# Kernel tuning notes

Hardware: AMD Instinct MI355X
Metric: run time of the kernel (lower is better)

The kernel has to match this reference:

```python
import jax, jax.numpy as jnp
import numpy as np

EPS = 1e-7  # K.epsilon()
ROUTINGS = 3


def squash(v, axis=-1):
    s2 = jnp.sum(jnp.square(v), axis=axis, keepdims=True)
    scale = s2 / (1.0 + s2) / jnp.sqrt(s2 + EPS)
    return scale * v


def setup_inputs() -> dict:
    key = jax.random.key(0)
    k1, k2 = jax.random.split(key)
    B, Ni, Di, No, Do = 64, 2048, 16, 32, 16
    inputs = jax.random.normal(k1, (B, Ni, Di), dtype=jnp.float32)
    # glorot-uniform-ish scale for W
    limit = np.sqrt(6.0 / (Di + Do)).astype(np.float32)
    W = jax.random.uniform(k2, (1, Ni, No, Do, Di), dtype=jnp.float32,
                           minval=-limit, maxval=limit)
    return {"inputs": inputs, "W": W}


def reference(inputs, W):
    # inputs: [B, Ni, Di]; W: [1, Ni, No, Do, Di]
    # inputs_hat[b,n,o,d] = sum_i W[n,o,d,i] * inputs[b,n,i]  -> [B, Ni, No, Do]
    inputs_hat = jnp.einsum('bni,nodi->bnod', inputs, W[0])
    B, Ni, No, _ = inputs_hat.shape
    b = jnp.zeros((B, Ni, No), dtype=inputs_hat.dtype)
    outputs = None
    for i in range(ROUTINGS):
        c = jax.nn.softmax(b, axis=2)              # [B, Ni, No]
        s = jnp.einsum('bnod,bno->bod', inputs_hat, c)  # weighted sum over Ni
        outputs = squash(s)                        # [B, No, Do]
        if i < ROUTINGS - 1:
            # NOTE: faithful to source — update uses sum over Do of c-weighted
            # inputs_hat (does NOT use `outputs`).
            b = b + jnp.sum(inputs_hat * c[..., None], axis=-1)
    return outputs
```

## Files before the change

kernel.cpp:

```cpp
#include <hip/hip_runtime.h>
#include <cmath>


#define NI 2048

typedef short bf16x8 __attribute__((ext_vector_type(8)));
typedef float f32x4 __attribute__((ext_vector_type(4)));

static __device__ __forceinline__ unsigned short f2bf(float f) {
  unsigned u = __float_as_uint(f);
  u += 0x7FFFu + ((u >> 16) & 1u);
  return (unsigned short)(u >> 16);
}
static __device__ __forceinline__ float bf2f(unsigned short h) {
  return __uint_as_float(((unsigned)h) << 16);
}
static __device__ __forceinline__ void split4(float4 v, uint2& hi, uint2& lo) {
  unsigned short h0 = f2bf(v.x), h1 = f2bf(v.y), h2 = f2bf(v.z), h3 = f2bf(v.w);
  unsigned short l0 = f2bf(v.x - bf2f(h0)), l1 = f2bf(v.y - bf2f(h1));
  unsigned short l2 = f2bf(v.z - bf2f(h2)), l3 = f2bf(v.w - bf2f(h3));
  hi.x = (unsigned)h0 | ((unsigned)h1 << 16); hi.y = (unsigned)h2 | ((unsigned)h3 << 16);
  lo.x = (unsigned)l0 | ((unsigned)l1 << 16); lo.y = (unsigned)l2 | ((unsigned)l3 << 16);
}

#define WAOFF 0
#define XBOFF 12288
#define HOFF  13056
#define C2OFF 14112
#define LDSZ  15168
__global__ __launch_bounds__(512, 4) void caps_fused_kernel(
    const float* __restrict__ x, const float* __restrict__ W,
    float* __restrict__ partial)
{
  const int bx = blockIdx.x;
  const int xcd = bx & 7, slot = bx >> 3;
  const int ng = xcd * 32 + (slot >> 1);
  const int bh = slot & 1;
  const int t = threadIdx.x;
  const int wv = t >> 6, l = t & 63;
  const int q = l >> 4, dq = l & 15, qh = q & 1, s_a = q >> 1;
  const int bt = wv & 1, oq = wv >> 1;

  __shared__ __align__(16) float lds[LDSZ];
  float* WA  = lds + WAOFF;
  float* XB  = lds + XBOFF;
  float* hS  = lds + HOFF;
  float* c2S = lds + C2OFF;

  float sacc[8][4];
  #pragma unroll
  for (int oo = 0; oo < 8; ++oo)
    { sacc[oo][0] = 0.f; sacc[oo][1] = 0.f; sacc[oo][2] = 0.f; sacc[oo][3] = 0.f; }

  const int n0 = ng * 8;
  const int wo0 = t >> 6, wd = (t >> 2) & 15, wi4 = t & 3;
  const int xb = t >> 2, xi4 = t & 3;

  float4 wreg[4];
  #pragma unroll
  for (int c = 0; c < 4; ++c)
    wreg[c] = *(const float4*)(W + (size_t)n0 * 8192 + c * 2048 + 4 * t);
  float4 xreg = make_float4(0.f, 0.f, 0.f, 0.f);
  if (t < 128)
    xreg = *(const float4*)(x + (size_t)(bh * 32 + xb) * (NI * 16) + n0 * 16 + xi4 * 4);

  #pragma unroll 1
  for (int nn = 0; nn < 8; ++nn) {
    #pragma unroll
    for (int c = 0; c < 4; ++c) {
      uint2 hi, lo;
      split4(wreg[c], hi, lo);
      const int row = ((c * 8 + wo0) * 32 + wd) * 12;
      *(uint2*)((char*)&WA[row] + wi4 * 8) = hi;
      *(uint2*)((char*)&WA[row + 192] + wi4 * 8) = lo;
    }
    if (t < 128) {
      uint2 hi, lo;
      split4(xreg, hi, lo);
      *(uint2*)((char*)&XB[xb * 12] + xi4 * 8) = hi;
      *(uint2*)((char*)&XB[(32 + xb) * 12] + xi4 * 8) = lo;
    }
    __syncthreads();

    if (nn < 7) {
      const size_t nb = (size_t)(n0 + nn + 1);
      #pragma unroll
      for (int c = 0; c < 4; ++c)
        wreg[c] = *(const float4*)(W + nb * 8192 + c * 2048 + 4 * t);
      if (t < 128)
        xreg = *(const float4*)(x + (size_t)(bh * 32 + xb) * (NI * 16) + nb * 16 + xi4 * 4);
    }

    f32x4 Dv[8];
    {
      bf16x8 B0 = *(const bf16x8*)&XB[(bt * 16 + dq) * 12 + qh * 4];
      bf16x8 B1 = *(const bf16x8*)&XB[(32 + bt * 16 + dq) * 12 + qh * 4];
      #pragma unroll
      for (int oo = 0; oo < 8; ++oo) {
        const int o = oq * 8 + oo;
        bf16x8 A = *(const bf16x8*)&WA[(o * 32 + s_a * 16 + dq) * 12 + qh * 4];
        f32x4 D = {0.f, 0.f, 0.f, 0.f};
        D = __builtin_amdgcn_mfma_f32_16x16x32_bf16(A, B0, D, 0, 0, 0);
        D = __builtin_amdgcn_mfma_f32_16x16x32_bf16(A, B1, D, 0, 0, 0);
        Dv[oo] = D;
        float hs = D[0] + D[1] + D[2] + D[3];
        hs += __shfl_xor(hs, 16);
        hs += __shfl_xor(hs, 32);
        if (q == 0) hS[(bt * 16 + dq) * 33 + o] = hs;
      }
    }
    __syncthreads();

    {
      const int bl = t >> 4, op = t & 15;
      const float h0 = hS[bl * 33 + op];
      const float h1 = hS[bl * 33 + op + 16];
      const float b10 = h0 * 0.03125f, b11 = h1 * 0.03125f;
      float mx = fmaxf(b10, b11);
      mx = fmaxf(mx, __shfl_xor(mx, 1)); mx = fmaxf(mx, __shfl_xor(mx, 2));
      mx = fmaxf(mx, __shfl_xor(mx, 4)); mx = fmaxf(mx, __shfl_xor(mx, 8));
      const float e0 = __expf(b10 - mx), e1 = __expf(b11 - mx);
      float S = e0 + e1;
      S += __shfl_xor(S, 1); S += __shfl_xor(S, 2);
      S += __shfl_xor(S, 4); S += __shfl_xor(S, 8);
      const float inv = 1.0f / S;
      const float b20 = b10 + e0 * inv * h0, b21 = b11 + e1 * inv * h1;
      float mx2 = fmaxf(b20, b21);
      mx2 = fmaxf(mx2, __shfl_xor(mx2, 1)); mx2 = fmaxf(mx2, __shfl_xor(mx2, 2));
      mx2 = fmaxf(mx2, __shfl_xor(mx2, 4)); mx2 = fmaxf(mx2, __shfl_xor(mx2, 8));
      const float e20 = __expf(b20 - mx2), e21 = __expf(b21 - mx2);
      float S2 = e20 + e21;
      S2 += __shfl_xor(S2, 1); S2 += __shfl_xor(S2, 2);
      S2 += __shfl_xor(S2, 4); S2 += __shfl_xor(S2, 8);
      const float inv2 = 1.0f / S2;
      c2S[op * 33 + bl] = e20 * inv2;
      c2S[(op + 16) * 33 + bl] = e21 * inv2;
    }
    __syncthreads();

    #pragma unroll
    for (int oo = 0; oo < 8; ++oo) {
      const int o = oq * 8 + oo;
      const float c = c2S[o * 33 + bt * 16 + dq];
      sacc[oo][0] += c * Dv[oo][0]; sacc[oo][1] += c * Dv[oo][1];
      sacc[oo][2] += c * Dv[oo][2]; sacc[oo][3] += c * Dv[oo][3];
    }
  }

  float* pb = partial + (size_t)ng * 32768
            + (size_t)(bh * 32 + bt * 16 + dq) * 512 + q * 4;
  #pragma unroll
  for (int oo = 0; oo < 8; ++oo) {
    const int o = oq * 8 + oo;
    *(float4*)(pb + o * 16)
        = make_float4(sacc[oo][0], sacc[oo][1], sacc[oo][2], sacc[oo][3]);
  }
}

__global__ __launch_bounds__(256) void caps_reduce_kernel(
    const float* __restrict__ partial, float* __restrict__ out)
{
  const int t = threadIdx.x;
  const int w4 = t >> 6, ln = t & 63;
  const int pair = blockIdx.x * 4 + w4;
  const int b = pair >> 5, o = pair & 31;
  const int d = ln & 15, cg = ln >> 4;
  const float* p = partial + (size_t)b * 512 + o * 16 + d;
  float s = 0.f;
  #pragma unroll 8
  for (int gg = cg; gg < 256; gg += 4) s += p[(size_t)gg * 32768];
  s += __shfl_xor(s, 16); s += __shfl_xor(s, 32);
  float s2 = s * s;
  s2 += __shfl_xor(s2, 1); s2 += __shfl_xor(s2, 2);
  s2 += __shfl_xor(s2, 4); s2 += __shfl_xor(s2, 8);
  float scale = s2 / (1.0f + s2) / sqrtf(s2 + 1e-7f);
  if (ln < 16) out[(size_t)b * 512 + o * 16 + d] = scale * s;
}

extern "C" void kernel_launch(void* const* d_in, const int* in_sizes, int n_in,
                              void* d_out, int out_size, void* d_ws, size_t ws_size,
                              hipStream_t stream) {
  const float* x = (const float*)d_in[0];
  const float* W = (const float*)d_in[1];
  if (in_sizes[0] != 64 * 2048 * 16) { const float* tmp = x; x = W; W = tmp; }
  float* out = (float*)d_out;

  float* partial = (float*)d_ws;

  caps_fused_kernel<<<512, 512, 0, stream>>>(x, W, partial);
  caps_reduce_kernel<<<512, 256, 0, stream>>>(partial, out);
}
```

Baseline: 126.7 us.

## Split batch into quarters per block, swizzle LDS layout, use packed bf16 convert

Each block now handles 16 batches instead of 32, which doubles the grid to 1024 blocks. LDS is shrunk and launch bounds are raised to 8 blocks per CU for higher occupancy. The hi/lo bf16 split now uses the v_cvt_pk_bf16_f32 instruction instead of manual rounding, and the LDS tiles use a compact XOR-swizzled 8-float row layout instead of padded 12-float rows. The trade-off is that every block reloads and re-splits the same W tile, so W traffic and conversion work double across the grid.

```diff
diff --git a/kernel.cpp b/kernel.cpp
--- a/kernel.cpp
+++ b/kernel.cpp
@@ -7,39 +7,41 @@
 typedef short bf16x8 __attribute__((ext_vector_type(8)));
 typedef float f32x4 __attribute__((ext_vector_type(4)));
 
-static __device__ __forceinline__ unsigned short f2bf(float f) {
-  unsigned u = __float_as_uint(f);
-  u += 0x7FFFu + ((u >> 16) & 1u);
-  return (unsigned short)(u >> 16);
+static __device__ __forceinline__ unsigned cvt_pk_bf16(float a, float b) {
+  unsigned r;
+  asm("v_cvt_pk_bf16_f32 %0, %1, %2" : "=v"(r) : "v"(a), "v"(b));
+  return r;
 }
-static __device__ __forceinline__ float bf2f(unsigned short h) {
-  return __uint_as_float(((unsigned)h) << 16);
+static __device__ __forceinline__ void split4_pk(float4 v, uint2& hi, uint2& lo) {
+  hi.x = cvt_pk_bf16(v.x, v.y);
+  hi.y = cvt_pk_bf16(v.z, v.w);
+  float r0 = v.x - __uint_as_float(hi.x << 16);
+  float r1 = v.y - __uint_as_float(hi.x & 0xFFFF0000u);
+  float r2 = v.z - __uint_as_float(hi.y << 16);
+  float r3 = v.w - __uint_as_float(hi.y & 0xFFFF0000u);
+  lo.x = cvt_pk_bf16(r0, r1);
+  lo.y = cvt_pk_bf16(r2, r3);
 }
-static __device__ __forceinline__ void split4(float4 v, uint2& hi, uint2& lo) {
-  unsigned short h0 = f2bf(v.x), h1 = f2bf(v.y), h2 = f2bf(v.z), h3 = f2bf(v.w);
-  unsigned short l0 = f2bf(v.x - bf2f(h0)), l1 = f2bf(v.y - bf2f(h1));
-  unsigned short l2 = f2bf(v.z - bf2f(h2)), l3 = f2bf(v.w - bf2f(h3));
-  hi.x = (unsigned)h0 | ((unsigned)h1 << 16); hi.y = (unsigned)h2 | ((unsigned)h3 << 16);
-  lo.x = (unsigned)l0 | ((unsigned)l1 << 16); lo.y = (unsigned)l2 | ((unsigned)l3 << 16);
+static __device__ __forceinline__ int swz8(int r, int u) {
+  return r * 8 + ((u ^ ((r >> 2) & 1)) << 2);
 }
 
 #define WAOFF 0
-#define XBOFF 12288
-#define HOFF  13056
-#define C2OFF 14112
-#define LDSZ  15168
-__global__ __launch_bounds__(512, 4) void caps_fused_kernel(
+#define XBOFF 8192
+#define HOFF  8448
+#define C2OFF 8976
+#define LDSZ  9520
+__global__ __launch_bounds__(512, 8) void caps_fused_kernel(
     const float* __restrict__ x, const float* __restrict__ W,
     float* __restrict__ partial)
 {
   const int bx = blockIdx.x;
   const int xcd = bx & 7, slot = bx >> 3;
-  const int ng = xcd * 32 + (slot >> 1);
-  const int bh = slot & 1;
+  const int ng = xcd * 32 + (slot >> 2);
+  const int bq = slot & 3;
   const int t = threadIdx.x;
   const int wv = t >> 6, l = t & 63;
   const int q = l >> 4, dq = l & 15, qh = q & 1, s_a = q >> 1;
-  const int bt = wv & 1, oq = wv >> 1;
 
   __shared__ __align__(16) float lds[LDSZ];
   float* WA  = lds + WAOFF;
@@ -47,38 +49,40 @@
   float* hS  = lds + HOFF;
   float* c2S = lds + C2OFF;
 
-  float sacc[8][4];
+  float sacc[4][4];
   #pragma unroll
-  for (int oo = 0; oo < 8; ++oo)
+  for (int oo = 0; oo < 4; ++oo)
     { sacc[oo][0] = 0.f; sacc[oo][1] = 0.f; sacc[oo][2] = 0.f; sacc[oo][3] = 0.f; }
 
   const int n0 = ng * 8;
-  const int wo0 = t >> 6, wd = (t >> 2) & 15, wi4 = t & 3;
+  const int wd = (t >> 2) & 15, wi4 = t & 3;
+  const int wu = wi4 >> 1, wsub = (wi4 & 1) * 2;
   const int xb = t >> 2, xi4 = t & 3;
+  const int xu = xi4 >> 1, xsub = (xi4 & 1) * 2;
 
   float4 wreg[4];
   #pragma unroll
   for (int c = 0; c < 4; ++c)
     wreg[c] = *(const float4*)(W + (size_t)n0 * 8192 + c * 2048 + 4 * t);
   float4 xreg = make_float4(0.f, 0.f, 0.f, 0.f);
-  if (t < 128)
-    xreg = *(const float4*)(x + (size_t)(bh * 32 + xb) * (NI * 16) + n0 * 16 + xi4 * 4);
+  if (t < 64)
+    xreg = *(const float4*)(x + (size_t)(bq * 16 + xb) * (NI * 16) + n0 * 16 + xi4 * 4);
 
   #pragma unroll 1
   for (int nn = 0; nn < 8; ++nn) {
     #pragma unroll
     for (int c = 0; c < 4; ++c) {
       uint2 hi, lo;
-      split4(wreg[c], hi, lo);
-      const int row = ((c * 8 + wo0) * 32 + wd) * 12;
-      *(uint2*)((char*)&WA[row] + wi4 * 8) = hi;
-      *(uint2*)((char*)&WA[row + 192] + wi4 * 8) = lo;
+      split4_pk(wreg[c], hi, lo);
+      const int rh = (c * 8 + wv) * 32 + wd;
+      *(uint2*)&WA[swz8(rh, wu) + wsub] = hi;
+      *(uint2*)&WA[swz8(rh + 16, wu) + wsub] = lo;
     }
-    if (t < 128) {
+    if (t < 64) {
       uint2 hi, lo;
-      split4(xreg, hi, lo);
-      *(uint2*)((char*)&XB[xb * 12] + xi4 * 8) = hi;
-      *(uint2*)((char*)&XB[(32 + xb) * 12] + xi4 * 8) = lo;
+      split4_pk(xreg, hi, lo);
+      *(uint2*)&XB[swz8(xb, xu) + xsub] = hi;
+      *(uint2*)&XB[swz8(16 + xb, xu) + xsub] = lo;
     }
     __syncthreads();
 
@@ -87,18 +91,18 @@
       #pragma unroll
       for (int c = 0; c < 4; ++c)
         wreg[c] = *(const float4*)(W + nb * 8192 + c * 2048 + 4 * t);
-      if (t < 128)
-        xreg = *(const float4*)(x + (size_t)(bh * 32 + xb) * (NI * 16) + nb * 16 + xi4 * 4);
+      if (t < 64)
+        xreg = *(const float4*)(x + (size_t)(bq * 16 + xb) * (NI * 16) + nb * 16 + xi4 * 4);
     }
 
-    f32x4 Dv[8];
+    f32x4 Dv[4];
     {
-      bf16x8 B0 = *(const bf16x8*)&XB[(bt * 16 + dq) * 12 + qh * 4];
-      bf16x8 B1 = *(const bf16x8*)&XB[(32 + bt * 16 + dq) * 12 + qh * 4];
+      bf16x8 B0 = *(const bf16x8*)&XB[swz8(dq, qh)];
+      bf16x8 B1 = *(const bf16x8*)&XB[swz8(16 + dq, qh)];
       #pragma unroll
-      for (int oo = 0; oo < 8; ++oo) {
-        const int o = oq * 8 + oo;
-        bf16x8 A = *(const bf16x8*)&WA[(o * 32 + s_a * 16 + dq) * 12 + qh * 4];
+      for (int oo = 0; oo < 4; ++oo) {
+        const int o = wv * 4 + oo;
+        bf16x8 A = *(const bf16x8*)&WA[swz8(o * 32 + s_a * 16 + dq, qh)];
         f32x4 D = {0.f, 0.f, 0.f, 0.f};
         D = __builtin_amdgcn_mfma_f32_16x16x32_bf16(A, B0, D, 0, 0, 0);
         D = __builtin_amdgcn_mfma_f32_16x16x32_bf16(A, B1, D, 0, 0, 0);
@@ -106,52 +110,50 @@
         float hs = D[0] + D[1] + D[2] + D[3];
         hs += __shfl_xor(hs, 16);
         hs += __shfl_xor(hs, 32);
-        if (q == 0) hS[(bt * 16 + dq) * 33 + o] = hs;
+        if (q == 0) hS[dq * 33 + o] = hs;
       }
     }
     __syncthreads();
 
     {
-      const int bl = t >> 4, op = t & 15;
-      const float h0 = hS[bl * 33 + op];
-      const float h1 = hS[bl * 33 + op + 16];
-      const float b10 = h0 * 0.03125f, b11 = h1 * 0.03125f;
-      float mx = fmaxf(b10, b11);
-      mx = fmaxf(mx, __shfl_xor(mx, 1)); mx = fmaxf(mx, __shfl_xor(mx, 2));
-      mx = fmaxf(mx, __shfl_xor(mx, 4)); mx = fmaxf(mx, __shfl_xor(mx, 8));
-      const float e0 = __expf(b10 - mx), e1 = __expf(b11 - mx);
-      float S = e0 + e1;
+      const int bl = t >> 5, o = t & 31;
+      const float h = hS[bl * 33 + o];
+      const float b1 = h * 0.03125f;
+      float mx = b1;
+      mx = fmaxf(mx, __shfl_xor(mx, 1));  mx = fmaxf(mx, __shfl_xor(mx, 2));
+      mx = fmaxf(mx, __shfl_xor(mx, 4));  mx = fmaxf(mx, __shfl_xor(mx, 8));
+      mx = fmaxf(mx, __shfl_xor(mx, 16));
+      const float e = __expf(b1 - mx);
+      float S = e;
       S += __shfl_xor(S, 1); S += __shfl_xor(S, 2);
-      S += __shfl_xor(S, 4); S += __shfl_xor(S, 8);
-      const float inv = 1.0f / S;
-      const float b20 = b10 + e0 * inv * h0, b21 = b11 + e1 * inv * h1;
-      float mx2 = fmaxf(b20, b21);
-      mx2 = fmaxf(mx2, __shfl_xor(mx2, 1)); mx2 = fmaxf(mx2, __shfl_xor(mx2, 2));
-      mx2 = fmaxf(mx2, __shfl_xor(mx2, 4)); mx2 = fmaxf(mx2, __shfl_xor(mx2, 8));
-      const float e20 = __expf(b20 - mx2), e21 = __expf(b21 - mx2);
-      float S2 = e20 + e21;
+      S += __shfl_xor(S, 4); S += __shfl_xor(S, 8); S += __shfl_xor(S, 16);
+      const float b2 = b1 + e * (1.0f / S) * h;
+      float mx2 = b2;
+      mx2 = fmaxf(mx2, __shfl_xor(mx2, 1));  mx2 = fmaxf(mx2, __shfl_xor(mx2, 2));
+      mx2 = fmaxf(mx2, __shfl_xor(mx2, 4));  mx2 = fmaxf(mx2, __shfl_xor(mx2, 8));
+      mx2 = fmaxf(mx2, __shfl_xor(mx2, 16));
+      const float e2 = __expf(b2 - mx2);
+      float S2 = e2;
       S2 += __shfl_xor(S2, 1); S2 += __shfl_xor(S2, 2);
-      S2 += __shfl_xor(S2, 4); S2 += __shfl_xor(S2, 8);
-      const float inv2 = 1.0f / S2;
-      c2S[op * 33 + bl] = e20 * inv2;
-      c2S[(op + 16) * 33 + bl] = e21 * inv2;
+      S2 += __shfl_xor(S2, 4); S2 += __shfl_xor(S2, 8); S2 += __shfl_xor(S2, 16);
+      c2S[o * 17 + bl] = e2 * (1.0f / S2);
     }
     __syncthreads();
 
     #pragma unroll
-    for (int oo = 0; oo < 8; ++oo) {
-      const int o = oq * 8 + oo;
-      const float c = c2S[o * 33 + bt * 16 + dq];
+    for (int oo = 0; oo < 4; ++oo) {
+      const int o = wv * 4 + oo;
+      const float c = c2S[o * 17 + dq];
       sacc[oo][0] += c * Dv[oo][0]; sacc[oo][1] += c * Dv[oo][1];
       sacc[oo][2] += c * Dv[oo][2]; sacc[oo][3] += c * Dv[oo][3];
     }
   }
 
   float* pb = partial + (size_t)ng * 32768
-            + (size_t)(bh * 32 + bt * 16 + dq) * 512 + q * 4;
+            + (size_t)(bq * 16 + dq) * 512 + q * 4;
   #pragma unroll
-  for (int oo = 0; oo < 8; ++oo) {
-    const int o = oq * 8 + oo;
+  for (int oo = 0; oo < 4; ++oo) {
+    const int o = wv * 4 + oo;
     *(float4*)(pb + o * 16)
         = make_float4(sacc[oo][0], sacc[oo][1], sacc[oo][2], sacc[oo][3]);
   }
@@ -187,6 +189,6 @@
 
   float* partial = (float*)d_ws;
 
-  caps_fused_kernel<<<512, 512, 0, stream>>>(x, W, partial);
+  caps_fused_kernel<<<1024, 512, 0, stream>>>(x, W, partial);
   caps_reduce_kernel<<<512, 256, 0, stream>>>(partial, out);
 }
```

After: 213.3 us. 68.4% more time.

## Pipeline LDS staging across iterations, swizzle bf16 layout, use packed bf16 convert

Applied to the files above, without the earlier changes.

Restructures the per-n loop so the next W/x slice is converted and written to LDS right after the MFMA phase, and the slice after that is loaded from global memory during the softmax phase. This removes one barrier-bounded staging step from each iteration's critical path. It also replaces the padded 12-float LDS rows with a compact XOR-swizzled 8-float layout to cut LDS footprint and bank conflicts. The hi/lo bf16 split now uses the v_cvt_pk_bf16_f32 instruction instead of manual rounding. Risks are higher register pressure from holding prefetched data across phases, and hazards from reusing the LDS buffers.

```diff
diff --git a/kernel.cpp b/kernel.cpp
--- a/kernel.cpp
+++ b/kernel.cpp
@@ -3,31 +3,36 @@
 
 
 #define NI 2048
+#define NGROUPS 256
+#define NPER 8
 
 typedef short bf16x8 __attribute__((ext_vector_type(8)));
 typedef float f32x4 __attribute__((ext_vector_type(4)));
 
-static __device__ __forceinline__ unsigned short f2bf(float f) {
-  unsigned u = __float_as_uint(f);
-  u += 0x7FFFu + ((u >> 16) & 1u);
-  return (unsigned short)(u >> 16);
-}
-static __device__ __forceinline__ float bf2f(unsigned short h) {
-  return __uint_as_float(((unsigned)h) << 16);
-}
-static __device__ __forceinline__ void split4(float4 v, uint2& hi, uint2& lo) {
-  unsigned short h0 = f2bf(v.x), h1 = f2bf(v.y), h2 = f2bf(v.z), h3 = f2bf(v.w);
-  unsigned short l0 = f2bf(v.x - bf2f(h0)), l1 = f2bf(v.y - bf2f(h1));
-  unsigned short l2 = f2bf(v.z - bf2f(h2)), l3 = f2bf(v.w - bf2f(h3));
-  hi.x = (unsigned)h0 | ((unsigned)h1 << 16); hi.y = (unsigned)h2 | ((unsigned)h3 << 16);
-  lo.x = (unsigned)l0 | ((unsigned)l1 << 16); lo.y = (unsigned)l2 | ((unsigned)l3 << 16);
+static __device__ __forceinline__ unsigned cvt_pk_bf16(float a, float b) {
+  unsigned r;
+  asm("v_cvt_pk_bf16_f32 %0, %1, %2" : "=v"(r) : "v"(a), "v"(b));
+  return r;
+}
+static __device__ __forceinline__ void split4_pk(float4 v, uint2& hi, uint2& lo) {
+  hi.x = cvt_pk_bf16(v.x, v.y);
+  hi.y = cvt_pk_bf16(v.z, v.w);
+  float r0 = v.x - __uint_as_float(hi.x << 16);
+  float r1 = v.y - __uint_as_float(hi.x & 0xFFFF0000u);
+  float r2 = v.z - __uint_as_float(hi.y << 16);
+  float r3 = v.w - __uint_as_float(hi.y & 0xFFFF0000u);
+  lo.x = cvt_pk_bf16(r0, r1);
+  lo.y = cvt_pk_bf16(r2, r3);
+}
+static __device__ __forceinline__ int swz8(int r, int u) {
+  return r * 8 + ((u ^ ((r >> 2) & 1)) << 2);
 }
 
 #define WAOFF 0
-#define XBOFF 12288
-#define HOFF  13056
-#define C2OFF 14112
-#define LDSZ  15168
+#define XBOFF 8192
+#define HOFF  8704
+#define C2OFF 9760
+#define LDSZ  10816
 __global__ __launch_bounds__(512, 4) void caps_fused_kernel(
     const float* __restrict__ x, const float* __restrict__ W,
     float* __restrict__ partial)
@@ -52,53 +57,55 @@
   for (int oo = 0; oo < 8; ++oo)
     { sacc[oo][0] = 0.f; sacc[oo][1] = 0.f; sacc[oo][2] = 0.f; sacc[oo][3] = 0.f; }
 
-  const int n0 = ng * 8;
-  const int wo0 = t >> 6, wd = (t >> 2) & 15, wi4 = t & 3;
+  const int n0 = ng * NPER;
+  const int wd = (t >> 2) & 15, wi4 = t & 3;
+  const int wu = wi4 >> 1, wsub = (wi4 & 1) * 2;
   const int xb = t >> 2, xi4 = t & 3;
+  const int xu = xi4 >> 1, xsub = (xi4 & 1) * 2;
 
   float4 wreg[4];
+  float4 xreg = make_float4(0.f, 0.f, 0.f, 0.f);
   #pragma unroll
   for (int c = 0; c < 4; ++c)
     wreg[c] = *(const float4*)(W + (size_t)n0 * 8192 + c * 2048 + 4 * t);
-  float4 xreg = make_float4(0.f, 0.f, 0.f, 0.f);
   if (t < 128)
     xreg = *(const float4*)(x + (size_t)(bh * 32 + xb) * (NI * 16) + n0 * 16 + xi4 * 4);
 
+  #pragma unroll
+  for (int c = 0; c < 4; ++c) {
+    uint2 hi, lo;
+    split4_pk(wreg[c], hi, lo);
+    const int rh = (c * 8 + wv) * 32 + wd;
+    *(uint2*)&WA[swz8(rh, wu) + wsub] = hi;
+    *(uint2*)&WA[swz8(rh + 16, wu) + wsub] = lo;
+  }
+  if (t < 128) {
+    uint2 hi, lo;
+    split4_pk(xreg, hi, lo);
+    *(uint2*)&XB[swz8(xb, xu) + xsub] = hi;
+    *(uint2*)&XB[swz8(32 + xb, xu) + xsub] = lo;
+  }
+  __syncthreads();
+
+  {
+    const size_t nb = (size_t)(n0 + 1);
+    #pragma unroll
+    for (int c = 0; c < 4; ++c)
+      wreg[c] = *(const float4*)(W + nb * 8192 + c * 2048 + 4 * t);
+    if (t < 128)
+      xreg = *(const float4*)(x + (size_t)(bh * 32 + xb) * (NI * 16) + nb * 16 + xi4 * 4);
+  }
+
   #pragma unroll 1
-  for (int nn = 0; nn < 8; ++nn) {
-    #pragma unroll
-    for (int c = 0; c < 4; ++c) {
-      uint2 hi, lo;
-      split4(wreg[c], hi, lo);
-      const int row = ((c * 8 + wo0) * 32 + wd) * 12;
-      *(uint2*)((char*)&WA[row] + wi4 * 8) = hi;
-      *(uint2*)((char*)&WA[row + 192] + wi4 * 8) = lo;
-    }
-    if (t < 128) {
-      uint2 hi, lo;
-      split4(xreg, hi, lo);
-      *(uint2*)((char*)&XB[xb * 12] + xi4 * 8) = hi;
-      *(uint2*)((char*)&XB[(32 + xb) * 12] + xi4 * 8) = lo;
-    }
-    __syncthreads();
-
-    if (nn < 7) {
-      const size_t nb = (size_t)(n0 + nn + 1);
-      #pragma unroll
-      for (int c = 0; c < 4; ++c)
-        wreg[c] = *(const float4*)(W + nb * 8192 + c * 2048 + 4 * t);
-      if (t < 128)
-        xreg = *(const float4*)(x + (size_t)(bh * 32 + xb) * (NI * 16) + nb * 16 + xi4 * 4);
-    }
-
+  for (int nn = 0; nn < NPER; ++nn) {
     f32x4 Dv[8];
     {
-      bf16x8 B0 = *(const bf16x8*)&XB[(bt * 16 + dq) * 12 + qh * 4];
-      bf16x8 B1 = *(const bf16x8*)&XB[(32 + bt * 16 + dq) * 12 + qh * 4];
+      bf16x8 B0 = *(const bf16x8*)&XB[swz8(bt * 16 + dq, qh)];
+      bf16x8 B1 = *(const bf16x8*)&XB[swz8(32 + bt * 16 + dq, qh)];
       #pragma unroll
       for (int oo = 0; oo < 8; ++oo) {
         const int o = oq * 8 + oo;
-        bf16x8 A = *(const bf16x8*)&WA[(o * 32 + s_a * 16 + dq) * 12 + qh * 4];
+        bf16x8 A = *(const bf16x8*)&WA[swz8(o * 32 + s_a * 16 + dq, qh)];
         f32x4 D = {0.f, 0.f, 0.f, 0.f};
         D = __builtin_amdgcn_mfma_f32_16x16x32_bf16(A, B0, D, 0, 0, 0);
         D = __builtin_amdgcn_mfma_f32_16x16x32_bf16(A, B1, D, 0, 0, 0);
@@ -110,6 +117,23 @@
       }
     }
     __syncthreads();
+
+    if (nn < NPER - 1) {
+      #pragma unroll
+      for (int c = 0; c < 4; ++c) {
+        uint2 hi, lo;
+        split4_pk(wreg[c], hi, lo);
+        const int rh = (c * 8 + wv) * 32 + wd;
+        *(uint2*)&WA[swz8(rh, wu) + wsub] = hi;
+        *(uint2*)&WA[swz8(rh + 16, wu) + wsub] = lo;
+      }
+      if (t < 128) {
+        uint2 hi, lo;
+        split4_pk(xreg, hi, lo);
+        *(uint2*)&XB[swz8(xb, xu) + xsub] = hi;
+        *(uint2*)&XB[swz8(32 + xb, xu) + xsub] = lo;
+      }
+    }
 
     {
       const int bl = t >> 4, op = t & 15;
@@ -136,6 +160,15 @@
       c2S[op * 33 + bl] = e20 * inv2;
       c2S[(op + 16) * 33 + bl] = e21 * inv2;
     }
+
+    if (nn < NPER - 2) {
+      const size_t nb = (size_t)(n0 + nn + 2);
+      #pragma unroll
+      for (int c = 0; c < 4; ++c)
+        wreg[c] = *(const float4*)(W + nb * 8192 + c * 2048 + 4 * t);
+      if (t < 128)
+        xreg = *(const float4*)(x + (size_t)(bh * 32 + xb) * (NI * 16) + nb * 16 + xi4 * 4);
+    }
     __syncthreads();
 
     #pragma unroll
@@ -168,7 +201,7 @@
   const float* p = partial + (size_t)b * 512 + o * 16 + d;
   float s = 0.f;
   #pragma unroll 8
-  for (int gg = cg; gg < 256; gg += 4) s += p[(size_t)gg * 32768];
+  for (int gg = cg; gg < NGROUPS; gg += 4) s += p[(size_t)gg * 32768];
   s += __shfl_xor(s, 16); s += __shfl_xor(s, 32);
   float s2 = s * s;
   s2 += __shfl_xor(s2, 1); s2 += __shfl_xor(s2, 2);
```

Measured after the change: 125.0 us. Within noise of the previous version (-1.3%).
